# Kernel optimization log

Hardware: AMD Instinct MI355X
Metric: run time of the kernel (lower is better)

Reference implementation:

```python
import jax, jax.numpy as jnp
import numpy as np

N_NODES = 200000
N_EDGES = 500000
F_IN = 165
HIDDEN = 384
OUT = 2


def setup_inputs() -> dict:
    key = jax.random.key(0)
    ks = jax.random.split(key, 8)
    x = jax.random.normal(ks[0], (N_NODES, F_IN), dtype=jnp.float32)
    edge_index = jax.random.randint(ks[1], (2, N_EDGES), 0, N_NODES, dtype=jnp.int64)
    # Glorot-ish init for GCNConv weights, zero bias (PyG default)
    def glorot(k, fan_in, fan_out):
        lim = (6.0 / (fan_in + fan_out)) ** 0.5
        return jax.random.uniform(k, (fan_in, fan_out), dtype=jnp.float32, minval=-lim, maxval=lim)
    W1 = glorot(ks[2], F_IN, HIDDEN)
    b1 = jnp.zeros((HIDDEN,), dtype=jnp.float32)
    W2 = glorot(ks[3], HIDDEN, HIDDEN)
    b2 = jnp.zeros((HIDDEN,), dtype=jnp.float32)
    W3 = glorot(ks[4], HIDDEN, OUT)
    b3 = jnp.zeros((OUT,), dtype=jnp.float32)
    return {"x": x, "edge_index": edge_index,
            "W1": W1, "b1": b1, "W2": W2, "b2": b2, "W3": W3, "b3": b3}


def _gcn_norm(edge_index, num_nodes):
    # PyG gcn_norm: add self-loops, symmetric normalization D^-1/2 (A+I) D^-1/2
    loop = jnp.arange(num_nodes, dtype=edge_index.dtype)
    row = jnp.concatenate([edge_index[0], loop])
    col = jnp.concatenate([edge_index[1], loop])
    ones = jnp.ones(row.shape[0], dtype=jnp.float32)
    deg = jax.ops.segment_sum(ones, col, num_segments=num_nodes)
    dinv = jnp.where(deg > 0, jax.lax.rsqrt(deg), 0.0)
    norm = dinv[row] * dinv[col]  # [E + N]
    return row, col, norm


def _gcn_conv(h, W, b, row, col, norm, num_nodes):
    h = h @ W                          # [N, F_out] linear transform first
    msg = h[row] * norm[:, None]       # gather + scale, [E+N, F_out]
    agg = jax.ops.segment_sum(msg, col, num_segments=num_nodes)
    return agg + b


def reference(x, edge_index, W1, b1, W2, b2, W3, b3):
    n = x.shape[0]
    row, col, norm = _gcn_norm(edge_index, n)
    h = jax.nn.relu(_gcn_conv(x, W1, b1, row, col, norm, n))
    h = jax.nn.relu(_gcn_conv(h, W2, b2, row, col, norm, n))
    return _gcn_conv(h, W3, b3, row, col, norm, n)
```

## Files before the change

kernel.cpp:

```cpp
#include <hip/hip_runtime.h>
#include <hip/hip_bf16.h>

#define N_NODES 200000
#define N_EDGES 500000
#define F_IN    165
#define HIDDEN  384
#define F_OUT   2

#define KPAD1   192
#define M_TILES 1563
#define M_PAD   (M_TILES * 128)
#define NB_SCAN 782

typedef unsigned short ushort_t;
typedef unsigned int   uint_t;

using bf16x8 = __attribute__((ext_vector_type(8))) short;
using f32x4  = __attribute__((ext_vector_type(4))) float;

__device__ __forceinline__ float bf2f(uint_t u) {
    return __uint_as_float(u << 16);
}
__device__ __forceinline__ ushort_t f2bf(float x) {
    uint_t b = __float_as_uint(x);
    return (ushort_t)((b + 0x7FFFu + ((b >> 16) & 1u)) >> 16);
}

__global__ void count_kernel(const int* __restrict__ col, int* __restrict__ cnt, int E) {
    int e = blockIdx.x * blockDim.x + threadIdx.x;
    if (e < E) atomicAdd(&cnt[col[e]], 1);
}

__global__ void dinv_kernel(const int* __restrict__ cnt, float* __restrict__ dinv, int n) {
    int i = blockIdx.x * blockDim.x + threadIdx.x;
    if (i < n) dinv[i] = rsqrtf((float)(cnt[i] + 1));
}

__global__ __launch_bounds__(256) void scan1_kernel(const int* __restrict__ cnt,
                                                    int* __restrict__ loc,
                                                    int* __restrict__ bsum, int N) {
    __shared__ int sh[256];
    int t = threadIdx.x;
    int i = blockIdx.x * 256 + t;
    int v = (i < N) ? cnt[i] : 0;
    sh[t] = v;
    __syncthreads();
    #pragma unroll
    for (int off = 1; off < 256; off <<= 1) {
        int u = (t >= off) ? sh[t - off] : 0;
        __syncthreads();
        sh[t] += u;
        __syncthreads();
    }
    int incl = sh[t];
    if (i < N) loc[i] = incl - v;
    if (t == 255) bsum[blockIdx.x] = incl;
}

__global__ __launch_bounds__(1024) void scan2_kernel(int* __restrict__ bsum, int NB) {
    __shared__ int sh[1024];
    int t = threadIdx.x;
    int v = (t < NB) ? bsum[t] : 0;
    sh[t] = v;
    __syncthreads();
    #pragma unroll
    for (int off = 1; off < 1024; off <<= 1) {
        int u = (t >= off) ? sh[t - off] : 0;
        __syncthreads();
        sh[t] += u;
        __syncthreads();
    }
    if (t < NB) bsum[t] = sh[t] - v;
}

__global__ __launch_bounds__(256) void scan3_kernel(int* __restrict__ ptr,
                                                    int* __restrict__ cursor,
                                                    const int* __restrict__ bsum,
                                                    int N, int E) {
    int t = threadIdx.x;
    int i = blockIdx.x * 256 + t;
    if (i < N) {
        int p = ptr[i] + bsum[blockIdx.x];
        ptr[i] = p;
        cursor[i] = p;
    }
    if (i == 0) ptr[N] = E;
}

__global__ void scatter_kernel(const int* __restrict__ row, const int* __restrict__ col,
                               const float* __restrict__ dinv,
                               int* __restrict__ cursor,
                               int* __restrict__ row_srt, float* __restrict__ nrm_srt, int E) {
    int e = blockIdx.x * blockDim.x + threadIdx.x;
    if (e >= E) return;
    int r = row[e], c = col[e];
    int pos = atomicAdd(&cursor[c], 1);
    row_srt[pos] = r;
    nrm_srt[pos] = dinv[r] * dinv[c];
}

__global__ void convx_kernel(const float* __restrict__ X, uint_t* __restrict__ Xb, int total) {
    int idx = blockIdx.x * blockDim.x + threadIdx.x;
    if (idx >= total) return;
    int node = idx / 96, ui = idx - node * 96;
    int f = ui * 2;
    const float* xr = X + (size_t)node * F_IN;
    float lo = (f < F_IN) ? xr[f] : 0.0f;
    float hi = (f + 1 < F_IN) ? xr[f + 1] : 0.0f;
    Xb[idx] = (uint_t)f2bf(lo) | ((uint_t)f2bf(hi) << 16);
}

__global__ __launch_bounds__(256) void agg165b_kernel(
        const uint_t* __restrict__ Xb, const float* __restrict__ dinv,
        const int* __restrict__ ptr, const int* __restrict__ row_srt,
        const float* __restrict__ nrm_srt, ushort_t* __restrict__ out, int N) {
    int w    = (blockIdx.x * blockDim.x + threadIdx.x) >> 6;
    int lane = threadIdx.x & 63;
    if (w >= N) return;
    float d2 = dinv[w]; d2 *= d2;
    const uint_t* self = Xb + (size_t)w * 96;
    bool two = (lane < 19);
    uint_t u0 = self[lane];
    uint_t u1 = two ? self[64 + lane] : 0u;
    float ax0 = bf2f(u0 & 0xFFFFu) * d2, ay0 = bf2f(u0 >> 16) * d2;
    float ax1 = bf2f(u1 & 0xFFFFu) * d2, ay1 = bf2f(u1 >> 16) * d2;
    int e0 = ptr[w], e1 = ptr[w + 1];
    for (int e = e0; e < e1; ++e) {
        int r = row_srt[e];
        float wg = nrm_srt[e];
        const uint_t* hr = Xb + (size_t)r * 96;
        uint_t v0 = hr[lane];
        uint_t v1 = two ? hr[64 + lane] : 0u;
        ax0 = fmaf(bf2f(v0 & 0xFFFFu), wg, ax0);
        ay0 = fmaf(bf2f(v0 >> 16), wg, ay0);
        ax1 = fmaf(bf2f(v1 & 0xFFFFu), wg, ax1);
        ay1 = fmaf(bf2f(v1 >> 16), wg, ay1);
    }
    uint_t* o = (uint_t*)(out + (size_t)w * KPAD1);
    o[lane] = (uint_t)f2bf(ax0) | ((uint_t)f2bf(ay0) << 16);
    if (two) o[64 + lane] = (uint_t)f2bf(ax1) | ((uint_t)f2bf(ay1) << 16);
}

__global__ __launch_bounds__(256) void agg384_kernel(
        const ushort_t* __restrict__ H, const float* __restrict__ dinv,
        const int* __restrict__ ptr, const int* __restrict__ row_srt,
        const float* __restrict__ nrm_srt, ushort_t* __restrict__ out, int N) {
    int w    = (blockIdx.x * blockDim.x + threadIdx.x) >> 6;
    int lane = threadIdx.x & 63;
    if (w >= N) return;
    float d2 = dinv[w]; d2 *= d2;
    const uint_t* self = (const uint_t*)(H + (size_t)w * HIDDEN);
    float ax[3], ay[3];
    #pragma unroll
    for (int j = 0; j < 3; ++j) {
        uint_t u = self[lane + 64 * j];
        ax[j] = bf2f(u & 0xFFFFu) * d2;
        ay[j] = bf2f(u >> 16) * d2;
    }
    int e0 = ptr[w], e1 = ptr[w + 1];
    for (int e = e0; e < e1; ++e) {
        int r = row_srt[e];
        float wg = nrm_srt[e];
        const uint_t* hr = (const uint_t*)(H + (size_t)r * HIDDEN);
        #pragma unroll
        for (int j = 0; j < 3; ++j) {
            uint_t u = hr[lane + 64 * j];
            ax[j] = fmaf(bf2f(u & 0xFFFFu), wg, ax[j]);
            ay[j] = fmaf(bf2f(u >> 16), wg, ay[j]);
        }
    }
    uint_t* o = (uint_t*)(out + (size_t)w * HIDDEN);
    #pragma unroll
    for (int j = 0; j < 3; ++j)
        o[lane + 64 * j] = (uint_t)f2bf(ax[j]) | ((uint_t)f2bf(ay[j]) << 16);
}

__global__ void prep_wt_kernel(const float* __restrict__ W, ushort_t* __restrict__ Wt,
                               int Kin, int Kpad, int Nn) {
    int idx = blockIdx.x * blockDim.x + threadIdx.x;
    if (idx >= Nn * Kpad) return;
    int n = idx / Kpad, k = idx - n * Kpad;
    float v = (k < Kin) ? W[(size_t)k * Nn + n] : 0.0f;
    Wt[idx] = f2bf(v);
}

#define GBK 32

template<bool RELU>
__global__ __launch_bounds__(256) void mfma_gemm_kernel(
        const ushort_t* __restrict__ A, const ushort_t* __restrict__ Wt,
        const float* __restrict__ bias, ushort_t* __restrict__ C,
        int Ks, int Nn) {
    __shared__ ushort_t As[128 * GBK];
    __shared__ ushort_t Bs[128 * GBK];

    const int tid  = threadIdx.x;
    const int lane = tid & 63;
    const int w    = tid >> 6;
    const int wm   = w & 1;
    const int wn   = w >> 1;
    const int bn   = blockIdx.x * 128;
    const int bm   = blockIdx.y * 128;

    const int rA = tid >> 2;
    const int q  = tid & 3;

    auto lds_off = [](int row, int chunk) {
        return row * GBK + ((chunk ^ ((row >> 1) & 3)) * 8);
    };
    const int wOff0 = lds_off(rA, q);
    const int wOff1 = lds_off(rA + 64, q);

    auto brow = [](int s) {
        return ((s >> 6) * 64) + ((s & 63) >> 4) + ((s & 15) * 4);
    };
    const int gB0 = brow(rA);
    const int gB1 = brow(rA + 64);

    const ushort_t* Ag0 = A  + (size_t)(bm + rA) * Ks + q * 8;
    const ushort_t* Ag1 = Ag0 + (size_t)64 * Ks;
    const ushort_t* Bg0 = Wt + (size_t)(bn + gB0) * Ks + q * 8;
    const ushort_t* Bg1 = Wt + (size_t)(bn + gB1) * Ks + q * 8;

    const int p     = lane & 15;
    const int khalf = lane >> 4;
    const int qf    = khalf ^ ((p >> 1) & 3);
    int aoff[4], boff[4];
    #pragma unroll
    for (int f = 0; f < 4; ++f) {
        aoff[f] = (wm * 64 + f * 16 + p) * GBK + qf * 8;
        boff[f] = (wn * 64 + f * 16 + p) * GBK + qf * 8;
    }

    f32x4 acc[4][4] = {};

    const int ksteps = Ks >> 5;
    for (int kt = 0; kt < ksteps; ++kt) {
        const int k0 = kt * GBK;
        uint4 va0 = *reinterpret_cast<const uint4*>(Ag0 + k0);
        uint4 va1 = *reinterpret_cast<const uint4*>(Ag1 + k0);
        uint4 vb0 = *reinterpret_cast<const uint4*>(Bg0 + k0);
        uint4 vb1 = *reinterpret_cast<const uint4*>(Bg1 + k0);
        *reinterpret_cast<uint4*>(&As[wOff0]) = va0;
        *reinterpret_cast<uint4*>(&As[wOff1]) = va1;
        *reinterpret_cast<uint4*>(&Bs[wOff0]) = vb0;
        *reinterpret_cast<uint4*>(&Bs[wOff1]) = vb1;
        __syncthreads();

        bf16x8 af[4], bfr[4];
        #pragma unroll
        for (int f = 0; f < 4; ++f) {
            af[f]  = *reinterpret_cast<const bf16x8*>(&As[aoff[f]]);
            bfr[f] = *reinterpret_cast<const bf16x8*>(&Bs[boff[f]]);
        }
        #pragma unroll
        for (int mi = 0; mi < 4; ++mi)
            #pragma unroll
            for (int ni = 0; ni < 4; ++ni)
                acc[mi][ni] = __builtin_amdgcn_mfma_f32_16x16x32_bf16(
                    af[mi], bfr[ni], acc[mi][ni], 0, 0, 0);
        __syncthreads();
    }

    const int colbase = bn + wn * 64 + p * 4;
    const float4 bb = *reinterpret_cast<const float4*>(bias + colbase);
    const float bias4[4] = {bb.x, bb.y, bb.z, bb.w};
    #pragma unroll
    for (int mi = 0; mi < 4; ++mi) {
        const int rowbase = bm + wm * 64 + mi * 16 + khalf * 4;
        #pragma unroll
        for (int j = 0; j < 4; ++j) {
            float v0 = acc[mi][0][j] + bias4[0];
            float v1 = acc[mi][1][j] + bias4[1];
            float v2 = acc[mi][2][j] + bias4[2];
            float v3 = acc[mi][3][j] + bias4[3];
            if (RELU) {
                v0 = fmaxf(v0, 0.f); v1 = fmaxf(v1, 0.f);
                v2 = fmaxf(v2, 0.f); v3 = fmaxf(v3, 0.f);
            }
            ushort4 o;
            o.x = f2bf(v0); o.y = f2bf(v1); o.z = f2bf(v2); o.w = f2bf(v3);
            *reinterpret_cast<ushort4*>(C + (size_t)(rowbase + j) * Nn + colbase) = o;
        }
    }
}

__global__ __launch_bounds__(256) void gemm_n2_kernel(
        const ushort_t* __restrict__ A, const float* __restrict__ W,
        float* __restrict__ G, int M) {
    int w    = (blockIdx.x * blockDim.x + threadIdx.x) >> 6;
    int lane = threadIdx.x & 63;
    if (w >= M) return;
    const uint_t* a = (const uint_t*)(A + (size_t)w * HIDDEN);
    float s0 = 0.f, s1 = 0.f;
    #pragma unroll
    for (int j = 0; j < 3; ++j) {
        int f2 = lane + 64 * j;
        uint_t u = a[f2];
        float alo = bf2f(u & 0xFFFFu), ahi = bf2f(u >> 16);
        int k = f2 * 2;
        s0 = fmaf(alo, W[k * 2 + 0], s0);
        s1 = fmaf(alo, W[k * 2 + 1], s1);
        s0 = fmaf(ahi, W[k * 2 + 2], s0);
        s1 = fmaf(ahi, W[k * 2 + 3], s1);
    }
    #pragma unroll
    for (int off = 32; off; off >>= 1) {
        s0 += __shfl_down(s0, off);
        s1 += __shfl_down(s1, off);
    }
    if (lane == 0) { G[(size_t)w * 2] = s0; G[(size_t)w * 2 + 1] = s1; }
}

__global__ void out_kernel(const float* __restrict__ G, const float* __restrict__ dinv,
                           const int* __restrict__ ptr, const int* __restrict__ row_srt,
                           const float* __restrict__ nrm_srt, const float* __restrict__ b3,
                           float* __restrict__ out, int N) {
    int i = blockIdx.x * blockDim.x + threadIdx.x;
    if (i >= N) return;
    float d2 = dinv[i]; d2 *= d2;
    float a0 = G[(size_t)i * 2 + 0] * d2 + b3[0];
    float a1 = G[(size_t)i * 2 + 1] * d2 + b3[1];
    int e0 = ptr[i], e1 = ptr[i + 1];
    for (int e = e0; e < e1; ++e) {
        int r = row_srt[e];
        float wg = nrm_srt[e];
        a0 = fmaf(G[(size_t)r * 2 + 0], wg, a0);
        a1 = fmaf(G[(size_t)r * 2 + 1], wg, a1);
    }
    out[(size_t)i * 2 + 0] = a0;
    out[(size_t)i * 2 + 1] = a1;
}

extern "C" void kernel_launch(void* const* d_in, const int* in_sizes, int n_in,
                              void* d_out, int out_size, void* d_ws, size_t ws_size,
                              hipStream_t stream) {
    const float* x   = (const float*)d_in[0];
    const int*   ei  = (const int*)  d_in[1];
    const float* W1  = (const float*)d_in[2];
    const float* b1  = (const float*)d_in[3];
    const float* W2  = (const float*)d_in[4];
    const float* b2  = (const float*)d_in[5];
    const float* W3  = (const float*)d_in[6];
    const float* b3  = (const float*)d_in[7];
    float* out = (float*)d_out;

    const int N = N_NODES, E = N_EDGES;
    const int* row = ei;
    const int* col = ei + E;

    size_t off = 0;
    auto alloc = [&](size_t bytes) { size_t o = off; off += (bytes + 255) & ~(size_t)255; return o; };
    size_t o_dinv   = alloc((size_t)N * 4);
    size_t o_ptr    = alloc((size_t)(N + 1) * 4);
    size_t o_cnt    = alloc((size_t)N * 4);
    size_t o_cursor = alloc((size_t)N * 4);
    size_t o_bsum   = alloc((size_t)NB_SCAN * 4);
    size_t o_rowsrt = alloc((size_t)E * 4);
    size_t o_nrmsrt = alloc((size_t)E * 4);
    size_t o_G      = alloc((size_t)N * 2 * 4);
    size_t o_Wt1    = alloc((size_t)HIDDEN * KPAD1 * 2);
    size_t o_Wt2    = alloc((size_t)HIDDEN * HIDDEN * 2);
    size_t o_B1     = alloc((size_t)M_PAD * HIDDEN * 2);
    size_t o_B2     = alloc((size_t)M_PAD * HIDDEN * 2);
    if (ws_size < off) return;

    char* ws = (char*)d_ws;
    float*    dinv    = (float*)(ws + o_dinv);
    int*      ptr     = (int*)  (ws + o_ptr);
    int*      cnt     = (int*)  (ws + o_cnt);
    int*      cursor  = (int*)  (ws + o_cursor);
    int*      bsum    = (int*)  (ws + o_bsum);
    int*      row_srt = (int*)  (ws + o_rowsrt);
    float*    nrm_srt = (float*)(ws + o_nrmsrt);
    float*    G       = (float*)(ws + o_G);
    ushort_t* Wt1     = (ushort_t*)(ws + o_Wt1);
    ushort_t* Wt2     = (ushort_t*)(ws + o_Wt2);
    ushort_t* B1      = (ushort_t*)(ws + o_B1);
    ushort_t* B2      = (ushort_t*)(ws + o_B2);
    uint_t*   Xb      = (uint_t*)B2;

    const int B = 256;

    prep_wt_kernel<<<(HIDDEN * KPAD1 + B - 1) / B, B, 0, stream>>>(W1, Wt1, F_IN, KPAD1, HIDDEN);
    prep_wt_kernel<<<(HIDDEN * HIDDEN + B - 1) / B, B, 0, stream>>>(W2, Wt2, HIDDEN, HIDDEN, HIDDEN);
    convx_kernel<<<(N * 96 + B - 1) / B, B, 0, stream>>>(x, Xb, N * 96);

    hipMemsetAsync(cnt, 0, (size_t)N * 4, stream);
    count_kernel<<<(E + B - 1) / B, B, 0, stream>>>(col, cnt, E);
    dinv_kernel<<<(N + B - 1) / B, B, 0, stream>>>(cnt, dinv, N);
    scan1_kernel<<<NB_SCAN, 256, 0, stream>>>(cnt, ptr, bsum, N);
    scan2_kernel<<<1, 1024, 0, stream>>>(bsum, NB_SCAN);
    scan3_kernel<<<NB_SCAN, 256, 0, stream>>>(ptr, cursor, bsum, N, E);
    scatter_kernel<<<(E + B - 1) / B, B, 0, stream>>>(row, col, dinv, cursor, row_srt, nrm_srt, E);

    agg165b_kernel<<<(N * 64 + B - 1) / B, B, 0, stream>>>(Xb, dinv, ptr, row_srt, nrm_srt, B1, N);

    {
        dim3 grid(HIDDEN / 128, M_TILES);
        mfma_gemm_kernel<true><<<grid, 256, 0, stream>>>(B1, Wt1, b1, B2, KPAD1, HIDDEN);
    }

    agg384_kernel<<<(N * 64 + B - 1) / B, B, 0, stream>>>(B2, dinv, ptr, row_srt, nrm_srt, B1, N);

    {
        dim3 grid(HIDDEN / 128, M_TILES);
        mfma_gemm_kernel<true><<<grid, 256, 0, stream>>>(B1, Wt2, b2, B2, HIDDEN, HIDDEN);
    }

    gemm_n2_kernel<<<(N * 64 + B - 1) / B, B, 0, stream>>>(B2, W3, G, N);

    out_kernel<<<(N + B - 1) / B, B, 0, stream>>>(G, dinv, ptr, row_srt, nrm_srt, b3, out, N);
}
```

Before: 539.8 us.

## Prefetch next GEMM k-tile into registers and remap block order for L2 reuse

```diff
diff --git a/kernel.cpp b/kernel.cpp
--- a/kernel.cpp
+++ b/kernel.cpp
@@ -11,6 +11,7 @@
 #define M_TILES 1563
 #define M_PAD   (M_TILES * 128)
 #define NB_SCAN 782
+#define GRID_GEMM (196 * 24)
 
 typedef unsigned short ushort_t;
 typedef unsigned int   uint_t;
@@ -190,17 +191,25 @@
 __global__ __launch_bounds__(256) void mfma_gemm_kernel(
         const ushort_t* __restrict__ A, const ushort_t* __restrict__ Wt,
         const float* __restrict__ bias, ushort_t* __restrict__ C,
-        int Ks, int Nn) {
+        int Ks, int Nn, int nTilesM) {
     __shared__ ushort_t As[128 * GBK];
     __shared__ ushort_t Bs[128 * GBK];
+
+    const int l  = blockIdx.x;
+    const int g  = l / 24;
+    const int r_ = l - g * 24;
+    const int cb = r_ >> 3;
+    const int pm = r_ & 7;
+    const int pt = g * 8 + pm;
+    if (pt >= nTilesM) return;
+    const int bm = pt * 128;
+    const int bn = cb * 128;
 
     const int tid  = threadIdx.x;
     const int lane = tid & 63;
     const int w    = tid >> 6;
     const int wm   = w & 1;
     const int wn   = w >> 1;
-    const int bn   = blockIdx.x * 128;
-    const int bm   = blockIdx.y * 128;
 
     const int rA = tid >> 2;
     const int q  = tid & 3;
@@ -235,17 +244,26 @@
     f32x4 acc[4][4] = {};
 
     const int ksteps = Ks >> 5;
+    uint4 va0 = *reinterpret_cast<const uint4*>(Ag0);
+    uint4 va1 = *reinterpret_cast<const uint4*>(Ag1);
+    uint4 vb0 = *reinterpret_cast<const uint4*>(Bg0);
+    uint4 vb1 = *reinterpret_cast<const uint4*>(Bg1);
+
     for (int kt = 0; kt < ksteps; ++kt) {
-        const int k0 = kt * GBK;
-        uint4 va0 = *reinterpret_cast<const uint4*>(Ag0 + k0);
-        uint4 va1 = *reinterpret_cast<const uint4*>(Ag1 + k0);
-        uint4 vb0 = *reinterpret_cast<const uint4*>(Bg0 + k0);
-        uint4 vb1 = *reinterpret_cast<const uint4*>(Bg1 + k0);
+        __syncthreads();
         *reinterpret_cast<uint4*>(&As[wOff0]) = va0;
         *reinterpret_cast<uint4*>(&As[wOff1]) = va1;
         *reinterpret_cast<uint4*>(&Bs[wOff0]) = vb0;
         *reinterpret_cast<uint4*>(&Bs[wOff1]) = vb1;
         __syncthreads();
+
+        if (kt + 1 < ksteps) {
+            const int k0 = (kt + 1) * GBK;
+            va0 = *reinterpret_cast<const uint4*>(Ag0 + k0);
+            va1 = *reinterpret_cast<const uint4*>(Ag1 + k0);
+            vb0 = *reinterpret_cast<const uint4*>(Bg0 + k0);
+            vb1 = *reinterpret_cast<const uint4*>(Bg1 + k0);
+        }
 
         bf16x8 af[4], bfr[4];
         #pragma unroll
@@ -259,7 +277,6 @@
             for (int ni = 0; ni < 4; ++ni)
                 acc[mi][ni] = __builtin_amdgcn_mfma_f32_16x16x32_bf16(
                     af[mi], bfr[ni], acc[mi][ni], 0, 0, 0);
-        __syncthreads();
     }
 
     const int colbase = bn + wn * 64 + p * 4;
@@ -396,17 +413,11 @@
 
     agg165b_kernel<<<(N * 64 + B - 1) / B, B, 0, stream>>>(Xb, dinv, ptr, row_srt, nrm_srt, B1, N);
 
-    {
-        dim3 grid(HIDDEN / 128, M_TILES);
-        mfma_gemm_kernel<true><<<grid, 256, 0, stream>>>(B1, Wt1, b1, B2, KPAD1, HIDDEN);
-    }
+    mfma_gemm_kernel<true><<<GRID_GEMM, 256, 0, stream>>>(B1, Wt1, b1, B2, KPAD1, HIDDEN, M_TILES);
 
     agg384_kernel<<<(N * 64 + B - 1) / B, B, 0, stream>>>(B2, dinv, ptr, row_srt, nrm_srt, B1, N);
 
-    {
-        dim3 grid(HIDDEN / 128, M_TILES);
-        mfma_gemm_kernel<true><<<grid, 256, 0, stream>>>(B1, Wt2, b2, B2, HIDDEN, HIDDEN);
-    }
+    mfma_gemm_kernel<true><<<GRID_GEMM, 256, 0, stream>>>(B1, Wt2, b2, B2, HIDDEN, HIDDEN, M_TILES);
 
     gemm_n2_kernel<<<(N * 64 + B - 1) / B, B, 0, stream>>>(B2, W3, G, N);
 
```

Result: faster. 508.4 us (-5.8%).
